# Kernel optimization log

Hardware: AMD Instinct MI355X
Metric: run time of the kernel (lower is better)

The kernel has to match this reference:

```python
import jax, jax.numpy as jnp
import numpy as np

B, H, P, K, E, BN = 8, 256, 1024, 32, 4, 64


def setup_inputs() -> dict:
    key = jax.random.key(0)
    ks = jax.random.split(key, 8)
    current = jax.random.normal(ks[0], (B, H, P), dtype=jnp.float32)
    neighbor_features = jax.random.normal(ks[1], (B, H, P, K), dtype=jnp.float32)
    # binary {0,1} validity mask, stored as float like the torch module expects
    neighbor_validity = jax.random.randint(ks[2], (B, 1, P, K), 0, 2).astype(jnp.float32)
    edge_features = jax.random.normal(ks[3], (B, E, P, K), dtype=jnp.float32)
    # 1x1 Conv2d weights flattened to matrices: (out_ch, in_ch)
    w1 = jax.random.normal(ks[4], (BN, 2 * H + E), dtype=jnp.float32) * 0.05
    b1 = jnp.zeros((BN,), dtype=jnp.float32)
    w2 = jax.random.normal(ks[5], (BN,), dtype=jnp.float32) * 0.05  # second conv: out_ch=1
    b2 = jnp.zeros((), dtype=jnp.float32)
    return {
        "current": current,
        "neighbor_features": neighbor_features,
        "neighbor_validity": neighbor_validity,
        "edge_features": edge_features,
        "w1": w1,
        "b1": b1,
        "w2": w2,
        "b2": b2,
    }


def reference(current, neighbor_features, neighbor_validity, edge_features, w1, b1, w2, b2):
    h_dim = current.shape[1]
    # Split the 1x1-conv weight along the concat axis so we never materialize
    # the [B, 2H+E, P, K] concatenated tensor (same math as cat + conv1x1).
    w1c = w1[:, :h_dim]            # acts on broadcast center features
    w1n = w1[:, h_dim:2 * h_dim]   # acts on neighbor features
    w1e = w1[:, 2 * h_dim:]        # acts on edge features

    hid = (
        jnp.einsum("bcp,oc->bop", current, w1c)[:, :, :, None]
        + jnp.einsum("bcpk,oc->bopk", neighbor_features, w1n)
        + jnp.einsum("bcpk,oc->bopk", edge_features, w1e)
        + b1[None, :, None, None]
    )
    hid = jax.nn.relu(hid)                                  # (B, BN, P, K)
    logits = jnp.einsum("bopk,o->bpk", hid, w2) + b2        # (B, P, K)

    valid = neighbor_validity[:, 0] > 0.5                   # (B, P, K) bool
    logits = jnp.where(valid, logits, -jnp.inf)
    has_any = jnp.any(valid, axis=-1, keepdims=True)        # (B, P, 1)
    logits_safe = jnp.where(has_any, logits, 0.0)           # all-masked rows -> 0 logits
    weights = jax.nn.softmax(logits_safe, axis=-1)
    weights = jnp.where(has_any & valid, weights, 0.0)      # zero weight on pads / empty rows

    pooled = jnp.einsum("bcpk,bpk->bcp", neighbor_features, weights)
    return pooled
```

## Files before the change

kernel.cpp:

```cpp
#include <hip/hip_runtime.h>
#include <math.h>


#define B_ 8
#define H_ 256
#define P_ 1024
#define K_ 32
#define E_ 4
#define BN_ 64

typedef __attribute__((ext_vector_type(8))) short short8;
typedef __attribute__((ext_vector_type(4))) float floatx4;

__device__ __forceinline__ unsigned short bf16_rne(float f) {
  unsigned u = __float_as_uint(f);
  u += 0x7fffu + ((u >> 16) & 1u);
  return (unsigned short)(u >> 16);
}
__device__ __forceinline__ unsigned pack_bf16_rne(float lo, float hi) {
  unsigned u0 = __float_as_uint(lo);
  u0 += 0x7fffu + ((u0 >> 16) & 1u);
  unsigned u1 = __float_as_uint(hi);
  u1 += 0x7fffu + ((u1 >> 16) & 1u);
  return (u0 >> 16) | (u1 & 0xffff0000u);
}

__global__ __launch_bounds__(256) void prep_kernel(
    const float* __restrict__ w1, unsigned short* __restrict__ w1m) {
  int i = blockIdx.x * 256 + threadIdx.x;
  if (i >= 4 * 17 * 64 * 8) return;
  int j = i & 7, lane = (i >> 3) & 63;
  int kt = i >> 9;
  int mt = kt / 17, ki = kt % 17;
  int o = mt * 16 + (lane & 15);
  int c = ki * 32 + (lane >> 4) * 8 + j;
  float v = (c < 516) ? w1[o * 516 + c] : 0.f;
  w1m[i] = bf16_rne(v);
}

__global__ __launch_bounds__(512, 2) void soft_attn_agg_kernel(
    const float* __restrict__ cur,
    const float* __restrict__ nf,
    const float* __restrict__ nv,
    const float* __restrict__ ef,
    const unsigned short* __restrict__ w1m,
    const float* __restrict__ b1,
    const float* __restrict__ w2,
    float* __restrict__ out) {
  __shared__ unsigned s_nf[256 * 132];
  __shared__ unsigned short s_curb[8][264];
  __shared__ unsigned s_edge[8][32][4];
  __shared__ float s_valid[256];
  __shared__ float s_b1v[BN_];
  __shared__ float s_w2v[BN_];
  __shared__ float s_lg[256];
  __shared__ float s_wt[256];

  const int t = threadIdx.x;
  const unsigned bid = blockIdx.x;
  const unsigned xcd = bid & 7u, sx = bid >> 3;
  const int b = (int)(sx >> 4);
  const int pg = (int)(xcd * 16u + (sx & 15u));
  const int p0 = pg * 8;

  const int w = t >> 6;
  const int lane = t & 63;
  const int q = lane >> 4;
  const int ln15 = lane & 15;

  {
    const int n = t & 255, ch = t >> 8;
    const float* gp = nf + (size_t)b * (H_ * P_ * K_) +
                      (size_t)(ch * 128) * (P_ * K_) + (size_t)p0 * K_ + n;
    unsigned* drow = s_nf + n * 132 + ch * 64;
#pragma unroll 4
    for (int i = 0; i < 16; ++i) {
      const float* gc = gp + (size_t)(8 * i) * (P_ * K_);
      float f0 = gc[0];
      float f1 = gc[(size_t)(P_ * K_)];
      float f2 = gc[(size_t)(2 * P_ * K_)];
      float f3 = gc[(size_t)(3 * P_ * K_)];
      float f4 = gc[(size_t)(4 * P_ * K_)];
      float f5 = gc[(size_t)(5 * P_ * K_)];
      float f6 = gc[(size_t)(6 * P_ * K_)];
      float f7 = gc[(size_t)(7 * P_ * K_)];
      uint4 d;
      d.x = pack_bf16_rne(f0, f1);
      d.y = pack_bf16_rne(f2, f3);
      d.z = pack_bf16_rne(f4, f5);
      d.w = pack_bf16_rne(f6, f7);
      *(uint4*)&drow[4 * i] = d;
    }
  }
  if (t < 256) {
    const float* cb = cur + ((size_t)b * H_ + t) * P_ + p0;
    float4 ca = *(const float4*)cb;
    float4 cc = *(const float4*)(cb + 4);
    s_curb[0][t] = bf16_rne(ca.x);
    s_curb[1][t] = bf16_rne(ca.y);
    s_curb[2][t] = bf16_rne(ca.z);
    s_curb[3][t] = bf16_rne(ca.w);
    s_curb[4][t] = bf16_rne(cc.x);
    s_curb[5][t] = bf16_rne(cc.y);
    s_curb[6][t] = bf16_rne(cc.z);
    s_curb[7][t] = bf16_rne(cc.w);
    s_valid[t] = nv[((size_t)b * P_ + p0) * K_ + t];
    const int pl = t >> 5, k = t & 31;
    const float* ep = ef + (size_t)b * (E_ * P_ * K_) + (size_t)p0 * K_ + t;
    float e0 = ep[0];
    float e1 = ep[(size_t)(P_ * K_)];
    float e2 = ep[(size_t)(2 * P_ * K_)];
    float e3 = ep[(size_t)(3 * P_ * K_)];
    uint4 d;
    d.x = pack_bf16_rne(e0, e1);
    d.y = pack_bf16_rne(e2, e3);
    d.z = 0u;
    d.w = 0u;
    *(uint4*)&s_edge[pl][k][0] = d;
  } else if (t < 320) {
    s_b1v[t - 256] = b1[t - 256];
  } else if (t < 384) {
    s_w2v[t - 320] = w2[t - 320];
  }
  __syncthreads();

  floatx4 acc[4][2];
#pragma unroll
  for (int mt = 0; mt < 4; ++mt) {
    floatx4 binit = *(const floatx4*)&s_b1v[mt * 16 + q * 4];
    acc[mt][0] = binit;
    acc[mt][1] = binit;
  }
  const unsigned short* w1m_l = w1m + (size_t)lane * 8;
  const int pl_w = w;

#pragma unroll
  for (int ki = 0; ki < 8; ++ki) {
    short8 bc = *(const short8*)&s_curb[pl_w][ki * 32 + q * 8];
#pragma unroll
    for (int mt = 0; mt < 4; ++mt) {
      short8 a = *(const short8*)(w1m_l + (size_t)(mt * 17 + ki) * 512);
      acc[mt][0] = __builtin_amdgcn_mfma_f32_16x16x32_bf16(a, bc, acc[mt][0], 0, 0, 0);
      acc[mt][1] = __builtin_amdgcn_mfma_f32_16x16x32_bf16(a, bc, acc[mt][1], 0, 0, 0);
    }
  }
#pragma unroll
  for (int ck = 0; ck < 8; ++ck) {
    short8 bn0 = *(const short8*)(s_nf + ((2 * w) * 16 + ln15) * 132 + 16 * ck + 4 * q);
    short8 bn1 = *(const short8*)(s_nf + ((2 * w + 1) * 16 + ln15) * 132 + 16 * ck + 4 * q);
#pragma unroll
    for (int mt = 0; mt < 4; ++mt) {
      short8 a = *(const short8*)(w1m_l + (size_t)(mt * 17 + 8 + ck) * 512);
      acc[mt][0] = __builtin_amdgcn_mfma_f32_16x16x32_bf16(a, bn0, acc[mt][0], 0, 0, 0);
      acc[mt][1] = __builtin_amdgcn_mfma_f32_16x16x32_bf16(a, bn1, acc[mt][1], 0, 0, 0);
    }
  }
  {
    short8 be0 = *(const short8*)&s_edge[pl_w][ln15][0];
    short8 be1 = *(const short8*)&s_edge[pl_w][16 + ln15][0];
#pragma unroll
    for (int mt = 0; mt < 4; ++mt) {
      short8 a = *(const short8*)(w1m_l + (size_t)(mt * 17 + 16) * 512);
      acc[mt][0] = __builtin_amdgcn_mfma_f32_16x16x32_bf16(a, be0, acc[mt][0], 0, 0, 0);
      acc[mt][1] = __builtin_amdgcn_mfma_f32_16x16x32_bf16(a, be1, acc[mt][1], 0, 0, 0);
    }
  }

#pragma unroll
  for (int nti = 0; nti < 2; ++nti) {
    float lp = 0.f;
#pragma unroll
    for (int mt = 0; mt < 4; ++mt) {
      const floatx4 w2v = *(const floatx4*)&s_w2v[mt * 16 + q * 4];
#pragma unroll
      for (int r = 0; r < 4; ++r)
        lp = fmaf(fmaxf(acc[mt][nti][r], 0.f), w2v[r], lp);
    }
    lp += __shfl_xor(lp, 16);
    lp += __shfl_xor(lp, 32);
    if (lane < 16) s_lg[(2 * w + nti) * 16 + ln15] = lp;
  }
  __syncthreads();

  if (t < 256) {
    float lg = s_lg[t];
    bool v = s_valid[t] > 0.5f;
    float ml = v ? lg : -INFINITY;
#pragma unroll
    for (int m = 1; m < 32; m <<= 1) ml = fmaxf(ml, __shfl_xor(ml, m));
    float e = v ? __expf(lg - ml) : 0.f;
    float ssum = e;
#pragma unroll
    for (int m = 1; m < 32; m <<= 1) ssum += __shfl_xor(ssum, m);
    s_wt[t] = (ml > -INFINITY) ? (e / ssum) : 0.f;
  }
  __syncthreads();

  {
    const int cpr = t & 127, ph = t >> 7;
    const int nb = ph * 64;
    float a0e = 0.f, a0o = 0.f, a1e = 0.f, a1o = 0.f;
#pragma unroll
    for (int k = 0; k < K_; ++k) {
      const unsigned u0 = s_nf[(nb + k) * 132 + cpr];
      const unsigned u1 = s_nf[(nb + 32 + k) * 132 + cpr];
      const float wt0 = s_wt[nb + k];
      const float wt1 = s_wt[nb + 32 + k];
      a0e = fmaf(__uint_as_float(u0 << 16), wt0, a0e);
      a0o = fmaf(__uint_as_float(u0 & 0xffff0000u), wt0, a0o);
      a1e = fmaf(__uint_as_float(u1 << 16), wt1, a1e);
      a1o = fmaf(__uint_as_float(u1 & 0xffff0000u), wt1, a1o);
    }
    float* op = out + ((size_t)b * H_ + 2 * cpr) * P_ + p0 + 2 * ph;
    float2 ve; ve.x = a0e; ve.y = a1e;
    float2 vo; vo.x = a0o; vo.y = a1o;
    *(float2*)op = ve;
    *(float2*)(op + P_) = vo;
  }
}

extern "C" void kernel_launch(void* const* d_in, const int* in_sizes, int n_in,
                              void* d_out, int out_size, void* d_ws,
                              size_t ws_size, hipStream_t stream) {
  const float* cur = (const float*)d_in[0];
  const float* nf  = (const float*)d_in[1];
  const float* nv  = (const float*)d_in[2];
  const float* ef  = (const float*)d_in[3];
  const float* w1  = (const float*)d_in[4];
  const float* b1  = (const float*)d_in[5];
  const float* w2  = (const float*)d_in[6];

  unsigned short* w1m = (unsigned short*)d_ws;
  prep_kernel<<<(4 * 17 * 64 * 8 + 255) / 256, 256, 0, stream>>>(w1, w1m);
  soft_attn_agg_kernel<<<B_ * P_ / 8, 512, 0, stream>>>(
      cur, nf, nv, ef, w1m, b1, w2, (float*)d_out);
}
```

Measured before the change: 408.1 us.

## Halve block tile and stage neighbor features via async global-to-LDS copies

Each block now handles 4 points with 256 threads instead of 8 points with 512, which halves shared-memory use so more blocks can be resident per CU. The neighbor-feature tile is no longer built from strided per-thread global loads packed in registers. Instead it streams through a small fp32 staging buffer using global_load_lds in 16 channel chunks, and each chunk is converted to packed bf16 in the main tile. The edge-feature slot shrinks to 2 words and is zero-padded in registers. The catch is a barrier per chunk, which serializes load latency. The staging buffer is also overwritten by the next chunk's async copies with no barrier after the reads, so there is a possible race.

```diff
diff --git a/kernel.cpp b/kernel.cpp
--- a/kernel.cpp
+++ b/kernel.cpp
@@ -23,6 +23,12 @@
   unsigned u1 = __float_as_uint(hi);
   u1 += 0x7fffu + ((u1 >> 16) & 1u);
   return (u0 >> 16) | (u1 & 0xffff0000u);
+}
+
+__device__ __forceinline__ void async_cp4(const float* g, float* l) {
+  __builtin_amdgcn_global_load_lds(
+      (const __attribute__((address_space(1))) unsigned*)g,
+      (__attribute__((address_space(3))) unsigned*)l, 4, 0, 0);
 }
 
 __global__ __launch_bounds__(256) void prep_kernel(
@@ -38,7 +44,7 @@
   w1m[i] = bf16_rne(v);
 }
 
-__global__ __launch_bounds__(512, 2) void soft_attn_agg_kernel(
+__global__ __launch_bounds__(256, 2) void soft_attn_agg_kernel(
     const float* __restrict__ cur,
     const float* __restrict__ nf,
     const float* __restrict__ nv,
@@ -47,21 +53,22 @@
     const float* __restrict__ b1,
     const float* __restrict__ w2,
     float* __restrict__ out) {
-  __shared__ unsigned s_nf[256 * 132];
-  __shared__ unsigned short s_curb[8][264];
-  __shared__ unsigned s_edge[8][32][4];
-  __shared__ float s_valid[256];
+  __shared__ unsigned s_tile[128 * 132];
+  __shared__ float s_raw[16 * 128];
+  __shared__ unsigned short s_curb[4][264];
+  __shared__ unsigned s_edge[4][32][2];
+  __shared__ float s_valid[128];
   __shared__ float s_b1v[BN_];
   __shared__ float s_w2v[BN_];
-  __shared__ float s_lg[256];
-  __shared__ float s_wt[256];
+  __shared__ float s_lg[128];
+  __shared__ float s_wt[128];
 
   const int t = threadIdx.x;
   const unsigned bid = blockIdx.x;
   const unsigned xcd = bid & 7u, sx = bid >> 3;
-  const int b = (int)(sx >> 4);
-  const int pg = (int)(xcd * 16u + (sx & 15u));
-  const int p0 = pg * 8;
+  const int b = (int)(sx >> 5);
+  const int pg = (int)(xcd * 32u + (sx & 31u));
+  const int p0 = pg * 4;
 
   const int w = t >> 6;
   const int lane = t & 63;
@@ -69,58 +76,52 @@
   const int ln15 = lane & 15;
 
   {
-    const int n = t & 255, ch = t >> 8;
-    const float* gp = nf + (size_t)b * (H_ * P_ * K_) +
-                      (size_t)(ch * 128) * (P_ * K_) + (size_t)p0 * K_ + n;
-    unsigned* drow = s_nf + n * 132 + ch * 64;
-#pragma unroll 4
-    for (int i = 0; i < 16; ++i) {
-      const float* gc = gp + (size_t)(8 * i) * (P_ * K_);
-      float f0 = gc[0];
-      float f1 = gc[(size_t)(P_ * K_)];
-      float f2 = gc[(size_t)(2 * P_ * K_)];
-      float f3 = gc[(size_t)(3 * P_ * K_)];
-      float f4 = gc[(size_t)(4 * P_ * K_)];
-      float f5 = gc[(size_t)(5 * P_ * K_)];
-      float f6 = gc[(size_t)(6 * P_ * K_)];
-      float f7 = gc[(size_t)(7 * P_ * K_)];
-      uint4 d;
-      d.x = pack_bf16_rne(f0, f1);
-      d.y = pack_bf16_rne(f2, f3);
-      d.z = pack_bf16_rne(f4, f5);
-      d.w = pack_bf16_rne(f6, f7);
-      *(uint4*)&drow[4 * i] = d;
-    }
-  }
-  if (t < 256) {
     const float* cb = cur + ((size_t)b * H_ + t) * P_ + p0;
     float4 ca = *(const float4*)cb;
-    float4 cc = *(const float4*)(cb + 4);
     s_curb[0][t] = bf16_rne(ca.x);
     s_curb[1][t] = bf16_rne(ca.y);
     s_curb[2][t] = bf16_rne(ca.z);
     s_curb[3][t] = bf16_rne(ca.w);
-    s_curb[4][t] = bf16_rne(cc.x);
-    s_curb[5][t] = bf16_rne(cc.y);
-    s_curb[6][t] = bf16_rne(cc.z);
-    s_curb[7][t] = bf16_rne(cc.w);
+  }
+  if (t < 128) {
     s_valid[t] = nv[((size_t)b * P_ + p0) * K_ + t];
     const int pl = t >> 5, k = t & 31;
-    const float* ep = ef + (size_t)b * (E_ * P_ * K_) + (size_t)p0 * K_ + t;
+    const float* ep = ef + ((size_t)b * E_ * P_ + p0 + pl) * K_ + k;
     float e0 = ep[0];
     float e1 = ep[(size_t)(P_ * K_)];
     float e2 = ep[(size_t)(2 * P_ * K_)];
     float e3 = ep[(size_t)(3 * P_ * K_)];
-    uint4 d;
-    d.x = pack_bf16_rne(e0, e1);
-    d.y = pack_bf16_rne(e2, e3);
-    d.z = 0u;
-    d.w = 0u;
-    *(uint4*)&s_edge[pl][k][0] = d;
-  } else if (t < 320) {
-    s_b1v[t - 256] = b1[t - 256];
-  } else if (t < 384) {
-    s_w2v[t - 320] = w2[t - 320];
+    s_edge[pl][k][0] = pack_bf16_rne(e0, e1);
+    s_edge[pl][k][1] = pack_bf16_rne(e2, e3);
+  } else if (t < 192) {
+    s_b1v[t - 128] = b1[t - 128];
+  } else {
+    s_w2v[t - 192] = w2[t - 192];
+  }
+
+  const float* nf_b = nf + ((size_t)b * H_ * P_ + p0) * K_;
+  for (int ch = 0; ch < 16; ++ch) {
+#pragma unroll
+    for (int r = 0; r < 4; ++r) {
+      const int cl = 4 * w + r;
+      const float* g = nf_b + (size_t)(ch * 16 + cl) * (P_ * K_);
+      float* l = &s_raw[cl * 128];
+      async_cp4(g + lane, l);
+      async_cp4(g + 64 + lane, l + 64);
+    }
+    __syncthreads();
+#pragma unroll
+    for (int j = 0; j < 2; ++j) {
+      const int r0 = 4 * w + 2 * j;
+      const int cp = ch * 8 + 2 * w + j;
+#pragma unroll
+      for (int i = 0; i < 2; ++i) {
+        const int n = lane + 64 * i;
+        float fe = s_raw[r0 * 128 + n];
+        float fo = s_raw[(r0 + 1) * 128 + n];
+        s_tile[n * 132 + cp] = pack_bf16_rne(fe, fo);
+      }
+    }
   }
   __syncthreads();
 
@@ -132,11 +133,10 @@
     acc[mt][1] = binit;
   }
   const unsigned short* w1m_l = w1m + (size_t)lane * 8;
-  const int pl_w = w;
 
 #pragma unroll
   for (int ki = 0; ki < 8; ++ki) {
-    short8 bc = *(const short8*)&s_curb[pl_w][ki * 32 + q * 8];
+    short8 bc = *(const short8*)&s_curb[w][ki * 32 + q * 8];
 #pragma unroll
     for (int mt = 0; mt < 4; ++mt) {
       short8 a = *(const short8*)(w1m_l + (size_t)(mt * 17 + ki) * 512);
@@ -146,8 +146,8 @@
   }
 #pragma unroll
   for (int ck = 0; ck < 8; ++ck) {
-    short8 bn0 = *(const short8*)(s_nf + ((2 * w) * 16 + ln15) * 132 + 16 * ck + 4 * q);
-    short8 bn1 = *(const short8*)(s_nf + ((2 * w + 1) * 16 + ln15) * 132 + 16 * ck + 4 * q);
+    short8 bn0 = *(const short8*)(s_tile + (32 * w + ln15) * 132 + 16 * ck + 4 * q);
+    short8 bn1 = *(const short8*)(s_tile + (32 * w + 16 + ln15) * 132 + 16 * ck + 4 * q);
 #pragma unroll
     for (int mt = 0; mt < 4; ++mt) {
       short8 a = *(const short8*)(w1m_l + (size_t)(mt * 17 + 8 + ck) * 512);
@@ -156,13 +156,16 @@
     }
   }
   {
-    short8 be0 = *(const short8*)&s_edge[pl_w][ln15][0];
-    short8 be1 = *(const short8*)&s_edge[pl_w][16 + ln15][0];
+    union { unsigned u[4]; short8 s; } ub0, ub1;
+    *(uint2*)&ub0.u[0] = *(const uint2*)&s_edge[w][ln15][0];
+    ub0.u[2] = 0u; ub0.u[3] = 0u;
+    *(uint2*)&ub1.u[0] = *(const uint2*)&s_edge[w][16 + ln15][0];
+    ub1.u[2] = 0u; ub1.u[3] = 0u;
 #pragma unroll
     for (int mt = 0; mt < 4; ++mt) {
       short8 a = *(const short8*)(w1m_l + (size_t)(mt * 17 + 16) * 512);
-      acc[mt][0] = __builtin_amdgcn_mfma_f32_16x16x32_bf16(a, be0, acc[mt][0], 0, 0, 0);
-      acc[mt][1] = __builtin_amdgcn_mfma_f32_16x16x32_bf16(a, be1, acc[mt][1], 0, 0, 0);
+      acc[mt][0] = __builtin_amdgcn_mfma_f32_16x16x32_bf16(a, ub0.s, acc[mt][0], 0, 0, 0);
+      acc[mt][1] = __builtin_amdgcn_mfma_f32_16x16x32_bf16(a, ub1.s, acc[mt][1], 0, 0, 0);
     }
   }
 
@@ -182,7 +185,7 @@
   }
   __syncthreads();
 
-  if (t < 256) {
+  if (t < 128) {
     float lg = s_lg[t];
     bool v = s_valid[t] > 0.5f;
     float ml = v ? lg : -INFINITY;
@@ -202,8 +205,8 @@
     float a0e = 0.f, a0o = 0.f, a1e = 0.f, a1o = 0.f;
 #pragma unroll
     for (int k = 0; k < K_; ++k) {
-      const unsigned u0 = s_nf[(nb + k) * 132 + cpr];
-      const unsigned u1 = s_nf[(nb + 32 + k) * 132 + cpr];
+      const unsigned u0 = s_tile[(nb + k) * 132 + cpr];
+      const unsigned u1 = s_tile[(nb + 32 + k) * 132 + cpr];
       const float wt0 = s_wt[nb + k];
       const float wt1 = s_wt[nb + 32 + k];
       a0e = fmaf(__uint_as_float(u0 << 16), wt0, a0e);
@@ -232,6 +235,6 @@
 
   unsigned short* w1m = (unsigned short*)d_ws;
   prep_kernel<<<(4 * 17 * 64 * 8 + 255) / 256, 256, 0, stream>>>(w1, w1m);
-  soft_attn_agg_kernel<<<B_ * P_ / 8, 512, 0, stream>>>(
+  soft_attn_agg_kernel<<<B_ * P_ / 4, 256, 0, stream>>>(
       cur, nf, nv, ef, w1m, b1, w2, (float*)d_out);
 }
```

Result: no change. 400.5 us (-1.9%).
